# Optimization experiments

Hardware: AMD Instinct MI355X
Metric: run time of the kernel (lower is better)

## Reference

```python
import jax, jax.numpy as jnp
import numpy as np

NUM_NODES = 20000
SEQ_LEN = 128
IN_FEATS = 2
HIDDEN = 32
N_TOTAL = NUM_NODES * SEQ_LEN  # flattened graph size
N_EDGES = 2_000_000


def setup_inputs() -> dict:
    key = jax.random.key(0)
    ks = jax.random.split(key, 10)
    x = jax.random.normal(ks[0], (NUM_NODES, SEQ_LEN, IN_FEATS), dtype=jnp.float32)
    edge_index = jax.random.randint(ks[1], (2, N_EDGES), 0, N_TOTAL, dtype=jnp.int64)
    s = 0.1
    gcn_W = jax.random.normal(ks[2], (IN_FEATS, HIDDEN), dtype=jnp.float32) * s
    gcn_b = jnp.zeros((HIDDEN,), dtype=jnp.float32)
    w_ih = jax.random.normal(ks[3], (4 * HIDDEN, HIDDEN), dtype=jnp.float32) * s
    w_hh = jax.random.normal(ks[4], (4 * HIDDEN, HIDDEN), dtype=jnp.float32) * s
    b_ih = jax.random.normal(ks[5], (4 * HIDDEN,), dtype=jnp.float32) * s
    b_hh = jax.random.normal(ks[6], (4 * HIDDEN,), dtype=jnp.float32) * s
    fc_W = jax.random.normal(ks[7], (HIDDEN, 1), dtype=jnp.float32) * s
    fc_b = jnp.zeros((1,), dtype=jnp.float32)
    return {"x": x, "edge_index": edge_index, "gcn_W": gcn_W, "gcn_b": gcn_b,
            "w_ih": w_ih, "w_hh": w_hh, "b_ih": b_ih, "b_hh": b_hh,
            "fc_W": fc_W, "fc_b": fc_b}


def _gcn(x_flat, edge_index, W, b):
    # PyG GCNConv: add self-loops, symmetric normalization, then linear+bias.
    src, dst = edge_index[0], edge_index[1]
    n = x_flat.shape[0]
    # degree at target side, including the self-loop (+1)
    deg = jax.ops.segment_sum(jnp.ones_like(dst, dtype=x_flat.dtype), dst, num_segments=n) + 1.0
    dinv = jax.lax.rsqrt(deg)  # deg >= 1 always (self-loop)
    h = x_flat @ W  # [n, HIDDEN] transform before propagate
    norm = dinv[src] * dinv[dst]  # [E]
    msg = h[src] * norm[:, None]  # gather + per-edge scale
    agg = jax.ops.segment_sum(msg, dst, num_segments=n)
    # self-loop contribution: dinv_i * dinv_i * h_i = h_i / deg_i
    out = agg + h * (1.0 / deg)[:, None]
    return out + b


def _lstm(xs, w_ih, w_hh, b_ih, b_hh):
    # torch LSTM gate order: i, f, g, o. xs: [N, S, H] -> final hidden [N, H]
    n, s, hdim = xs.shape
    xs_t = jnp.swapaxes(xs, 0, 1)  # [S, N, H]
    # precompute input projections once (dense GEMM)
    x_proj = xs_t @ w_ih.T + b_ih + b_hh  # [S, N, 4H]

    def step(carry, xp):
        h, c = carry
        g = xp + h @ w_hh.T  # [N, 4H]
        i, f, gg, o = jnp.split(g, 4, axis=-1)
        c = jax.nn.sigmoid(f) * c + jax.nn.sigmoid(i) * jnp.tanh(gg)
        h = jax.nn.sigmoid(o) * jnp.tanh(c)
        return (h, c), None

    h0 = jnp.zeros((n, hdim), dtype=xs.dtype)
    (hn, _), _ = jax.lax.scan(step, (h0, h0), x_proj)
    return hn


def reference(x, edge_index, gcn_W, gcn_b, w_ih, w_hh, b_ih, b_hh, fc_W, fc_b):
    num_nodes, seq_len, num_feats = x.shape
    x_in = x.reshape(-1, num_feats)  # [N*S, F]
    x_gcn = jax.nn.relu(_gcn(x_in, edge_index, gcn_W, gcn_b))
    x_lstm = x_gcn.reshape(num_nodes, seq_len, -1)
    hn = _lstm(x_lstm, w_ih, w_hh, b_ih, b_hh)
    return hn @ fc_W + fc_b  # [num_nodes, 1]
```

## Files before the change

### kernel.cpp

```cpp
#include <hip/hip_runtime.h>

#define SEQ 128
#define HID 32

typedef __attribute__((ext_vector_type(8))) short short8;
typedef __attribute__((ext_vector_type(4))) float floatx4;


__global__ void count_kernel(const int* __restrict__ idx, int E, int* __restrict__ cnt) {
    int e = (blockIdx.x * blockDim.x + threadIdx.x) * 4;
    if (((E & 3) == 0) && e + 3 < E) {
        int4 d = *(const int4*)(idx + E + e);
        atomicAdd(&cnt[d.x], 1);
        atomicAdd(&cnt[d.y], 1);
        atomicAdd(&cnt[d.z], 1);
        atomicAdd(&cnt[d.w], 1);
    } else {
        int lim = min(e + 4, E);
        for (int k = e; k < lim; ++k) atomicAdd(&cnt[idx[E + k]], 1);
    }
}

__device__ __forceinline__ unsigned long long pk2(float xx, float yy, float dv) {
    int qx = __float2int_rn(xx * dv * 2097152.0f);
    int qy = __float2int_rn(yy * dv * 2097152.0f);
    return ((unsigned long long)(unsigned)(qx + (1 << 26)) << 32) |
           (unsigned)(qy + (1 << 26));
}

__global__ void scatter_pk_kernel(const int* __restrict__ idx, int E,
                                  const float2* __restrict__ x2,
                                  const int* __restrict__ deg,
                                  unsigned long long* __restrict__ aggP) {
    int e = (blockIdx.x * blockDim.x + threadIdx.x) * 4;
    if (((E & 3) == 0) && e + 3 < E) {
        int4 s = *(const int4*)(idx + e);
        int4 d = *(const int4*)(idx + E + e);
        float2 v0 = x2[s.x];
        float2 v1 = x2[s.y];
        float2 v2 = x2[s.z];
        float2 v3 = x2[s.w];
        float dv0 = rsqrtf((float)deg[s.x] + 1.0f);
        float dv1 = rsqrtf((float)deg[s.y] + 1.0f);
        float dv2 = rsqrtf((float)deg[s.z] + 1.0f);
        float dv3 = rsqrtf((float)deg[s.w] + 1.0f);
        atomicAdd(&aggP[d.x], pk2(v0.x, v0.y, dv0));
        atomicAdd(&aggP[d.y], pk2(v1.x, v1.y, dv1));
        atomicAdd(&aggP[d.z], pk2(v2.x, v2.y, dv2));
        atomicAdd(&aggP[d.w], pk2(v3.x, v3.y, dv3));
    } else {
        int lim = min(e + 4, E);
        for (int k = e; k < lim; ++k) {
            int s = idx[k];
            int d = idx[E + k];
            float2 v = x2[s];
            float dv = rsqrtf((float)deg[s] + 1.0f);
            atomicAdd(&aggP[d], pk2(v.x, v.y, dv));
        }
    }
}


__device__ __forceinline__ float sigm_f(float x) {
    return __builtin_amdgcn_rcpf(1.0f + __expf(-x));
}
__device__ __forceinline__ float tanh_f(float x) {
    return fmaf(__builtin_amdgcn_rcpf(1.0f + __expf(-2.0f * x)), 2.0f, -1.0f);
}
__device__ __forceinline__ void fsplit(float f, short& hi, short& lo) {
    unsigned u = __float_as_uint(f);
    hi = (short)(u >> 16);
    float r = f - __uint_as_float(u & 0xFFFF0000u);
    lo = (short)(__float_as_uint(r) >> 16);
}

__global__ __launch_bounds__(64, 1) void lstm_sw_kernel(
    const float2* __restrict__ x2,
    const unsigned long long* __restrict__ aggP, const int* __restrict__ deg,
    int N,
    const float* __restrict__ gcn_W, const float* __restrict__ gcn_b,
    const float* __restrict__ w_ih, const float* __restrict__ w_hh,
    const float* __restrict__ b_ih, const float* __restrict__ b_hh,
    const float* __restrict__ fc_W, const float* __restrict__ fc_b,
    float* __restrict__ out) {
    __shared__ float2 ubuf[16][SEQ + 1];

    const int lane = threadIdx.x;
    const int n = lane & 15;
    const int qq = lane >> 4;
    const int base = blockIdx.x * 16;

    {
        const float2* xb = x2 + (size_t)base * SEQ;
        const unsigned long long* apb = aggP + (size_t)base * SEQ;
        const int* dgb = deg + (size_t)base * SEQ;
        const int lim = min(16 * SEQ, (N - base) * SEQ);
        #pragma unroll 4
        for (int i = lane; i < 16 * SEQ; i += 64) {
            float2 v = make_float2(0.f, 0.f);
            if (i < lim) {
                int dg = dgb[i];
                float dv = rsqrtf((float)dg + 1.0f);
                float2 xx = xb[i];
                unsigned long long pk = apb[i];
                unsigned bias = (unsigned)dg * 67108864u;
                float ax = (float)((int)((unsigned)(pk >> 32) - bias)) * (1.0f / 2097152.0f);
                float ay = (float)((int)((unsigned)pk - bias)) * (1.0f / 2097152.0f);
                v = make_float2(dv * fmaf(xx.x, dv, ax), dv * fmaf(xx.y, dv, ay));
            }
            ubuf[i >> 7][i & 127] = v;
        }
        if (lane < 16) ubuf[lane][SEQ] = make_float2(0.f, 0.f);
    }

    short8 AiH[4][2], AiL[4][2], AhH[4][2], AhL[4][2];
    floatx4 biasC[4][2];
    #pragma unroll
    for (int g = 0; g < 4; ++g) {
        #pragma unroll
        for (int t1 = 0; t1 < 2; ++t1) {
            const int arow = g * 32 + 8 * (n >> 2) + 4 * t1 + (n & 3);
            const float* wi = w_ih + arow * HID + 8 * qq;
            const float* wh = w_hh + arow * HID + 8 * qq;
            #pragma unroll
            for (int j = 0; j < 8; ++j) {
                short h16, l16;
                fsplit(wi[j], h16, l16); AiH[g][t1][j] = h16; AiL[g][t1][j] = l16;
                fsplit(wh[j], h16, l16); AhH[g][t1][j] = h16; AhL[g][t1][j] = l16;
            }
            #pragma unroll
            for (int r = 0; r < 4; ++r) {
                const int brow = g * 32 + 8 * qq + 4 * t1 + r;
                biasC[g][t1][r] = b_ih[brow] + b_hh[brow];
            }
        }
    }

    float wg0[8], wg1[8], gbc[8], fcw[8];
    #pragma unroll
    for (int j = 0; j < 8; ++j) {
        const int u = 8 * qq + j;
        wg0[j] = gcn_W[u];
        wg1[j] = gcn_W[HID + u];
        gbc[j] = gcn_b[u];
        fcw[j] = fc_W[u];
    }

    float c[2][4], ho[2][4];
    #pragma unroll
    for (int t1 = 0; t1 < 2; ++t1)
        #pragma unroll
        for (int r = 0; r < 4; ++r) { c[t1][r] = 0.f; ho[t1][r] = 0.f; }

    short8 hh = (short8){0, 0, 0, 0, 0, 0, 0, 0};
    short8 hl = (short8){0, 0, 0, 0, 0, 0, 0, 0};
    short8 xh, xl;
    floatx4 aX[4][2];

    {
        float2 uu = ubuf[n][0];
        #pragma unroll
        for (int j = 0; j < 8; ++j) {
            float g = fmaxf(fmaf(uu.x, wg0[j], fmaf(uu.y, wg1[j], gbc[j])), 0.f);
            short h16, l16;
            fsplit(g, h16, l16);
            xh[j] = h16; xl[j] = l16;
        }
    }
    #pragma unroll
    for (int g = 0; g < 4; ++g)
        #pragma unroll
        for (int t1 = 0; t1 < 2; ++t1)
            aX[g][t1] = __builtin_amdgcn_mfma_f32_16x16x32_bf16(AiH[g][t1], xh, biasC[g][t1], 0, 0, 0);
    #pragma unroll
    for (int g = 0; g < 4; ++g)
        #pragma unroll
        for (int t1 = 0; t1 < 2; ++t1)
            aX[g][t1] = __builtin_amdgcn_mfma_f32_16x16x32_bf16(AiL[g][t1], xh, aX[g][t1], 0, 0, 0);
    #pragma unroll
    for (int g = 0; g < 4; ++g)
        #pragma unroll
        for (int t1 = 0; t1 < 2; ++t1)
            aX[g][t1] = __builtin_amdgcn_mfma_f32_16x16x32_bf16(AiH[g][t1], xl, aX[g][t1], 0, 0, 0);

    #pragma unroll 1
    for (int t = 0; t < SEQ; ++t) {
        floatx4 acc[4][2];
        #pragma unroll
        for (int g = 0; g < 4; ++g)
            #pragma unroll
            for (int t1 = 0; t1 < 2; ++t1)
                acc[g][t1] = __builtin_amdgcn_mfma_f32_16x16x32_bf16(AhH[g][t1], hh, aX[g][t1], 0, 0, 0);
        #pragma unroll
        for (int g = 0; g < 4; ++g)
            #pragma unroll
            for (int t1 = 0; t1 < 2; ++t1)
                acc[g][t1] = __builtin_amdgcn_mfma_f32_16x16x32_bf16(AhL[g][t1], hh, acc[g][t1], 0, 0, 0);
        #pragma unroll
        for (int g = 0; g < 4; ++g)
            #pragma unroll
            for (int t1 = 0; t1 < 2; ++t1)
                acc[g][t1] = __builtin_amdgcn_mfma_f32_16x16x32_bf16(AhH[g][t1], hl, acc[g][t1], 0, 0, 0);

        {
            float2 uu = ubuf[n][t + 1];
            #pragma unroll
            for (int j = 0; j < 8; ++j) {
                float g = fmaxf(fmaf(uu.x, wg0[j], fmaf(uu.y, wg1[j], gbc[j])), 0.f);
                short h16, l16;
                fsplit(g, h16, l16);
                xh[j] = h16; xl[j] = l16;
            }
        }
        #pragma unroll
        for (int g = 0; g < 4; ++g)
            #pragma unroll
            for (int t1 = 0; t1 < 2; ++t1)
                aX[g][t1] = __builtin_amdgcn_mfma_f32_16x16x32_bf16(AiH[g][t1], xh, biasC[g][t1], 0, 0, 0);
        #pragma unroll
        for (int g = 0; g < 4; ++g)
            #pragma unroll
            for (int t1 = 0; t1 < 2; ++t1)
                aX[g][t1] = __builtin_amdgcn_mfma_f32_16x16x32_bf16(AiL[g][t1], xh, aX[g][t1], 0, 0, 0);
        #pragma unroll
        for (int g = 0; g < 4; ++g)
            #pragma unroll
            for (int t1 = 0; t1 < 2; ++t1)
                aX[g][t1] = __builtin_amdgcn_mfma_f32_16x16x32_bf16(AiH[g][t1], xl, aX[g][t1], 0, 0, 0);

        #pragma unroll
        for (int t1 = 0; t1 < 2; ++t1) {
            #pragma unroll
            for (int r = 0; r < 4; ++r) {
                const float ig = sigm_f(acc[0][t1][r]);
                const float fg = sigm_f(acc[1][t1][r]);
                const float gg = tanh_f(acc[2][t1][r]);
                const float og = sigm_f(acc[3][t1][r]);
                c[t1][r] = fmaf(fg, c[t1][r], ig * gg);
                const float hv = og * tanh_f(c[t1][r]);
                ho[t1][r] = hv;
                short h16, l16;
                fsplit(hv, h16, l16);
                hh[4 * t1 + r] = h16;
                hl[4 * t1 + r] = l16;
            }
        }
    }

    float partial = 0.f;
    #pragma unroll
    for (int t1 = 0; t1 < 2; ++t1)
        #pragma unroll
        for (int r = 0; r < 4; ++r)
            partial = fmaf(ho[t1][r], fcw[4 * t1 + r], partial);
    partial += __shfl_xor(partial, 16);
    partial += __shfl_xor(partial, 32);
    if (lane < 16) {
        const int node = base + n;
        if (node < N) out[node] = partial + fc_b[0];
    }
}

extern "C" void kernel_launch(void* const* d_in, const int* in_sizes, int n_in,
                              void* d_out, int out_size, void* d_ws, size_t ws_size,
                              hipStream_t stream) {
    const float* x     = (const float*)d_in[0];
    const int*   idx   = (const int*)d_in[1];
    const float* gcn_W = (const float*)d_in[2];
    const float* gcn_b = (const float*)d_in[3];
    const float* w_ih  = (const float*)d_in[4];
    const float* w_hh  = (const float*)d_in[5];
    const float* b_ih  = (const float*)d_in[6];
    const float* b_hh  = (const float*)d_in[7];
    const float* fc_W  = (const float*)d_in[8];
    const float* fc_b  = (const float*)d_in[9];

    const int num_nodes = in_sizes[0] / (SEQ * 2);
    const int ntot = num_nodes * SEQ;
    const int E = in_sizes[1] / 2;

    int* deg = (int*)d_ws;
    unsigned long long* aggP = (unsigned long long*)((char*)d_ws + (size_t)ntot * 4);

    hipMemsetAsync(d_ws, 0, (size_t)ntot * 12, stream);

    const int eb = (E + 1023) / 1024;
    count_kernel<<<eb, 256, 0, stream>>>(idx, E, deg);
    scatter_pk_kernel<<<eb, 256, 0, stream>>>(idx, E, (const float2*)x, deg, aggP);
    lstm_sw_kernel<<<(num_nodes + 15) / 16, 64, 0, stream>>>(
        (const float2*)x, aggP, deg, num_nodes,
        gcn_W, gcn_b, w_ih, w_hh, b_ih, b_hh, fc_W, fc_b,
        (float*)d_out);
}
```

Measured before the change: 542.3 us.

## Split LSTM gates across four waves per block with LDS exchange of state

Each 16-node block now runs four wavefronts instead of one, and each wave computes one gate's MFMA tiles. Gate activations go through shared memory, and each wave updates a 2-hidden-unit slice of the cell and hidden state, written back to LDS for the next step's recurrent MFMA. This cuts the serial MFMA and transcendental chain per step by spreading it over more waves. The cost is two block-wide barriers per timestep plus LDS round trips. MFMA issue is also raised in priority with s_setprio.

```diff
diff --git a/kernel.cpp b/kernel.cpp
--- a/kernel.cpp
+++ b/kernel.cpp
@@ -2,6 +2,8 @@
 
 #define SEQ 128
 #define HID 32
+#define TPB 256
+#define XS 56
 
 typedef __attribute__((ext_vector_type(8))) short short8;
 typedef __attribute__((ext_vector_type(4))) float floatx4;
@@ -73,8 +75,11 @@
     float r = f - __uint_as_float(u & 0xFFFF0000u);
     lo = (short)(__float_as_uint(r) >> 16);
 }
-
-__global__ __launch_bounds__(64, 1) void lstm_sw_kernel(
+__device__ __forceinline__ int pks(short a, short b) {
+    return (int)(((unsigned)(unsigned short)b << 16) | (unsigned short)a);
+}
+
+__global__ __launch_bounds__(TPB, 4) void lstm_gs_kernel(
     const float2* __restrict__ x2,
     const unsigned long long* __restrict__ aggP, const int* __restrict__ deg,
     int N,
@@ -84,10 +89,18 @@
     const float* __restrict__ fc_W, const float* __restrict__ fc_b,
     float* __restrict__ out) {
     __shared__ float2 ubuf[16][SEQ + 1];
-
-    const int lane = threadIdx.x;
+    __shared__ float pre[4][32][17];
+    __shared__ __align__(16) short hhb[16][XS];
+    __shared__ __align__(16) short hlb[16][XS];
+    __shared__ __align__(16) short xgb[16][XS];
+    __shared__ __align__(16) short xlb[16][XS];
+    __shared__ float fcp[4][16];
+
+    const int tid = threadIdx.x;
+    const int w = tid >> 6;
+    const int lane = tid & 63;
     const int n = lane & 15;
-    const int qq = lane >> 4;
+    const int q = lane >> 4;
     const int base = blockIdx.x * 16;
 
     {
@@ -95,8 +108,7 @@
         const unsigned long long* apb = aggP + (size_t)base * SEQ;
         const int* dgb = deg + (size_t)base * SEQ;
         const int lim = min(16 * SEQ, (N - base) * SEQ);
-        #pragma unroll 4
-        for (int i = lane; i < 16 * SEQ; i += 64) {
+        for (int i = tid; i < 16 * SEQ; i += TPB) {
             float2 v = make_float2(0.f, 0.f);
             if (i < lim) {
                 int dg = dgb[i];
@@ -110,154 +122,156 @@
             }
             ubuf[i >> 7][i & 127] = v;
         }
-        if (lane < 16) ubuf[lane][SEQ] = make_float2(0.f, 0.f);
-    }
-
-    short8 AiH[4][2], AiL[4][2], AhH[4][2], AhL[4][2];
-    floatx4 biasC[4][2];
+        if (tid < 16) ubuf[tid][SEQ] = make_float2(0.f, 0.f);
+    }
+
+    short8 AiH[2], AiL[2], AhH[2], AhL[2];
+    floatx4 biasC[2];
     #pragma unroll
-    for (int g = 0; g < 4; ++g) {
-        #pragma unroll
-        for (int t1 = 0; t1 < 2; ++t1) {
-            const int arow = g * 32 + 8 * (n >> 2) + 4 * t1 + (n & 3);
-            const float* wi = w_ih + arow * HID + 8 * qq;
-            const float* wh = w_hh + arow * HID + 8 * qq;
-            #pragma unroll
-            for (int j = 0; j < 8; ++j) {
-                short h16, l16;
-                fsplit(wi[j], h16, l16); AiH[g][t1][j] = h16; AiL[g][t1][j] = l16;
-                fsplit(wh[j], h16, l16); AhH[g][t1][j] = h16; AhL[g][t1][j] = l16;
-            }
-            #pragma unroll
-            for (int r = 0; r < 4; ++r) {
-                const int brow = g * 32 + 8 * qq + 4 * t1 + r;
-                biasC[g][t1][r] = b_ih[brow] + b_hh[brow];
-            }
-        }
-    }
-
-    float wg0[8], wg1[8], gbc[8], fcw[8];
-    #pragma unroll
-    for (int j = 0; j < 8; ++j) {
-        const int u = 8 * qq + j;
-        wg0[j] = gcn_W[u];
-        wg1[j] = gcn_W[HID + u];
-        gbc[j] = gcn_b[u];
-        fcw[j] = fc_W[u];
-    }
-
-    float c[2][4], ho[2][4];
-    #pragma unroll
-    for (int t1 = 0; t1 < 2; ++t1)
-        #pragma unroll
-        for (int r = 0; r < 4; ++r) { c[t1][r] = 0.f; ho[t1][r] = 0.f; }
-
-    short8 hh = (short8){0, 0, 0, 0, 0, 0, 0, 0};
-    short8 hl = (short8){0, 0, 0, 0, 0, 0, 0, 0};
-    short8 xh, xl;
-    floatx4 aX[4][2];
-
+    for (int t1 = 0; t1 < 2; ++t1) {
+        const int arow = w * 32 + 16 * t1 + n;
+        const float* wi = w_ih + arow * HID + 8 * q;
+        const float* wh = w_hh + arow * HID + 8 * q;
+        #pragma unroll
+        for (int j = 0; j < 8; ++j) {
+            short h16, l16;
+            fsplit(wi[j], h16, l16); AiH[t1][j] = h16; AiL[t1][j] = l16;
+            fsplit(wh[j], h16, l16); AhH[t1][j] = h16; AhL[t1][j] = l16;
+        }
+        #pragma unroll
+        for (int r = 0; r < 4; ++r) {
+            const int brow = w * 32 + 16 * t1 + 4 * q + r;
+            biasC[t1][r] = b_ih[brow] + b_hh[brow];
+        }
+    }
+
+    const int ua = 8 * w + 2 * q;
+    const float wg0a = gcn_W[ua],       wg0b = gcn_W[ua + 1];
+    const float wg1a = gcn_W[HID + ua], wg1b = gcn_W[HID + ua + 1];
+    const float gbca = gcn_b[ua],       gbcb = gcn_b[ua + 1];
+    const float fcwa = fc_W[ua],        fcwb = fc_W[ua + 1];
+
+    float c0 = 0.f, c1 = 0.f, ho0 = 0.f, ho1 = 0.f;
+
+    __syncthreads();
+
+    *(int*)&hhb[n][ua] = 0;
+    *(int*)&hlb[n][ua] = 0;
     {
         float2 uu = ubuf[n][0];
-        #pragma unroll
-        for (int j = 0; j < 8; ++j) {
-            float g = fmaxf(fmaf(uu.x, wg0[j], fmaf(uu.y, wg1[j], gbc[j])), 0.f);
-            short h16, l16;
-            fsplit(g, h16, l16);
-            xh[j] = h16; xl[j] = l16;
-        }
-    }
-    #pragma unroll
-    for (int g = 0; g < 4; ++g)
+        float ga = fmaxf(fmaf(uu.x, wg0a, fmaf(uu.y, wg1a, gbca)), 0.f);
+        float gb = fmaxf(fmaf(uu.x, wg0b, fmaf(uu.y, wg1b, gbcb)), 0.f);
+        short gah, gal, gbh, gbl;
+        fsplit(ga, gah, gal); fsplit(gb, gbh, gbl);
+        *(int*)&xgb[n][ua] = pks(gah, gbh);
+        *(int*)&xlb[n][ua] = pks(gal, gbl);
+    }
+    __syncthreads();
+
+    floatx4 aX[2];
+    {
+        const short8 xh = *(const short8*)&xgb[n][8 * q];
+        const short8 xl = *(const short8*)&xlb[n][8 * q];
+        __builtin_amdgcn_s_setprio(1);
         #pragma unroll
         for (int t1 = 0; t1 < 2; ++t1)
-            aX[g][t1] = __builtin_amdgcn_mfma_f32_16x16x32_bf16(AiH[g][t1], xh, biasC[g][t1], 0, 0, 0);
-    #pragma unroll
-    for (int g = 0; g < 4; ++g)
+            aX[t1] = __builtin_amdgcn_mfma_f32_16x16x32_bf16(AiH[t1], xh, biasC[t1], 0, 0, 0);
         #pragma unroll
         for (int t1 = 0; t1 < 2; ++t1)
-            aX[g][t1] = __builtin_amdgcn_mfma_f32_16x16x32_bf16(AiL[g][t1], xh, aX[g][t1], 0, 0, 0);
-    #pragma unroll
-    for (int g = 0; g < 4; ++g)
+            aX[t1] = __builtin_amdgcn_mfma_f32_16x16x32_bf16(AiL[t1], xh, aX[t1], 0, 0, 0);
         #pragma unroll
         for (int t1 = 0; t1 < 2; ++t1)
-            aX[g][t1] = __builtin_amdgcn_mfma_f32_16x16x32_bf16(AiH[g][t1], xl, aX[g][t1], 0, 0, 0);
+            aX[t1] = __builtin_amdgcn_mfma_f32_16x16x32_bf16(AiH[t1], xl, aX[t1], 0, 0, 0);
+        __builtin_amdgcn_s_setprio(0);
+    }
 
     #pragma unroll 1
     for (int t = 0; t < SEQ; ++t) {
-        floatx4 acc[4][2];
-        #pragma unroll
-        for (int g = 0; g < 4; ++g)
-            #pragma unroll
-            for (int t1 = 0; t1 < 2; ++t1)
-                acc[g][t1] = __builtin_amdgcn_mfma_f32_16x16x32_bf16(AhH[g][t1], hh, aX[g][t1], 0, 0, 0);
-        #pragma unroll
-        for (int g = 0; g < 4; ++g)
-            #pragma unroll
-            for (int t1 = 0; t1 < 2; ++t1)
-                acc[g][t1] = __builtin_amdgcn_mfma_f32_16x16x32_bf16(AhL[g][t1], hh, acc[g][t1], 0, 0, 0);
-        #pragma unroll
-        for (int g = 0; g < 4; ++g)
-            #pragma unroll
-            for (int t1 = 0; t1 < 2; ++t1)
-                acc[g][t1] = __builtin_amdgcn_mfma_f32_16x16x32_bf16(AhH[g][t1], hl, acc[g][t1], 0, 0, 0);
-
         {
+            const short8 hh = *(const short8*)&hhb[n][8 * q];
+            const short8 hl = *(const short8*)&hlb[n][8 * q];
+            floatx4 acc[2];
+            __builtin_amdgcn_s_setprio(1);
+            #pragma unroll
+            for (int t1 = 0; t1 < 2; ++t1)
+                acc[t1] = __builtin_amdgcn_mfma_f32_16x16x32_bf16(AhH[t1], hh, aX[t1], 0, 0, 0);
+            #pragma unroll
+            for (int t1 = 0; t1 < 2; ++t1)
+                acc[t1] = __builtin_amdgcn_mfma_f32_16x16x32_bf16(AhL[t1], hh, acc[t1], 0, 0, 0);
+            #pragma unroll
+            for (int t1 = 0; t1 < 2; ++t1)
+                acc[t1] = __builtin_amdgcn_mfma_f32_16x16x32_bf16(AhH[t1], hl, acc[t1], 0, 0, 0);
+            __builtin_amdgcn_s_setprio(0);
+            float av[8];
+            #pragma unroll
+            for (int t1 = 0; t1 < 2; ++t1)
+                #pragma unroll
+                for (int r = 0; r < 4; ++r) av[4 * t1 + r] = acc[t1][r];
+            if (w == 2) {
+                #pragma unroll
+                for (int k = 0; k < 8; ++k) av[k] = tanh_f(av[k]);
+            } else {
+                #pragma unroll
+                for (int k = 0; k < 8; ++k) av[k] = sigm_f(av[k]);
+            }
+            #pragma unroll
+            for (int t1 = 0; t1 < 2; ++t1)
+                #pragma unroll
+                for (int r = 0; r < 4; ++r)
+                    pre[w][16 * t1 + 4 * q + r][n] = av[4 * t1 + r];
+        }
+        __syncthreads();
+
+        {
+            const float i0 = pre[0][ua][n],     f0 = pre[1][ua][n];
+            const float g0 = pre[2][ua][n],     o0 = pre[3][ua][n];
+            const float i1 = pre[0][ua + 1][n], f1 = pre[1][ua + 1][n];
+            const float g1 = pre[2][ua + 1][n], o1 = pre[3][ua + 1][n];
+            c0 = fmaf(f0, c0, i0 * g0);
+            c1 = fmaf(f1, c1, i1 * g1);
+            const float h0 = o0 * tanh_f(c0);
+            const float h1 = o1 * tanh_f(c1);
+            ho0 = h0; ho1 = h1;
+            short h0h, h0l, h1h, h1l;
+            fsplit(h0, h0h, h0l); fsplit(h1, h1h, h1l);
+            *(int*)&hhb[n][ua] = pks(h0h, h1h);
+            *(int*)&hlb[n][ua] = pks(h0l, h1l);
             float2 uu = ubuf[n][t + 1];
-            #pragma unroll
-            for (int j = 0; j < 8; ++j) {
-                float g = fmaxf(fmaf(uu.x, wg0[j], fmaf(uu.y, wg1[j], gbc[j])), 0.f);
-                short h16, l16;
-                fsplit(g, h16, l16);
-                xh[j] = h16; xl[j] = l16;
-            }
-        }
-        #pragma unroll
-        for (int g = 0; g < 4; ++g)
-            #pragma unroll
-            for (int t1 = 0; t1 < 2; ++t1)
-                aX[g][t1] = __builtin_amdgcn_mfma_f32_16x16x32_bf16(AiH[g][t1], xh, biasC[g][t1], 0, 0, 0);
-        #pragma unroll
-        for (int g = 0; g < 4; ++g)
-            #pragma unroll
-            for (int t1 = 0; t1 < 2; ++t1)
-                aX[g][t1] = __builtin_amdgcn_mfma_f32_16x16x32_bf16(AiL[g][t1], xh, aX[g][t1], 0, 0, 0);
-        #pragma unroll
-        for (int g = 0; g < 4; ++g)
-            #pragma unroll
-            for (int t1 = 0; t1 < 2; ++t1)
-                aX[g][t1] = __builtin_amdgcn_mfma_f32_16x16x32_bf16(AiH[g][t1], xl, aX[g][t1], 0, 0, 0);
-
-        #pragma unroll
-        for (int t1 = 0; t1 < 2; ++t1) {
-            #pragma unroll
-            for (int r = 0; r < 4; ++r) {
-                const float ig = sigm_f(acc[0][t1][r]);
-                const float fg = sigm_f(acc[1][t1][r]);
-                const float gg = tanh_f(acc[2][t1][r]);
-                const float og = sigm_f(acc[3][t1][r]);
-                c[t1][r] = fmaf(fg, c[t1][r], ig * gg);
-                const float hv = og * tanh_f(c[t1][r]);
-                ho[t1][r] = hv;
-                short h16, l16;
-                fsplit(hv, h16, l16);
-                hh[4 * t1 + r] = h16;
-                hl[4 * t1 + r] = l16;
-            }
-        }
-    }
-
-    float partial = 0.f;
-    #pragma unroll
-    for (int t1 = 0; t1 < 2; ++t1)
-        #pragma unroll
-        for (int r = 0; r < 4; ++r)
-            partial = fmaf(ho[t1][r], fcw[4 * t1 + r], partial);
+            float ga = fmaxf(fmaf(uu.x, wg0a, fmaf(uu.y, wg1a, gbca)), 0.f);
+            float gb = fmaxf(fmaf(uu.x, wg0b, fmaf(uu.y, wg1b, gbcb)), 0.f);
+            short gah, gal, gbh, gbl;
+            fsplit(ga, gah, gal); fsplit(gb, gbh, gbl);
+            *(int*)&xgb[n][ua] = pks(gah, gbh);
+            *(int*)&xlb[n][ua] = pks(gal, gbl);
+        }
+        __syncthreads();
+
+        {
+            const short8 xh = *(const short8*)&xgb[n][8 * q];
+            const short8 xl = *(const short8*)&xlb[n][8 * q];
+            __builtin_amdgcn_s_setprio(1);
+            #pragma unroll
+            for (int t1 = 0; t1 < 2; ++t1)
+                aX[t1] = __builtin_amdgcn_mfma_f32_16x16x32_bf16(AiH[t1], xh, biasC[t1], 0, 0, 0);
+            #pragma unroll
+            for (int t1 = 0; t1 < 2; ++t1)
+                aX[t1] = __builtin_amdgcn_mfma_f32_16x16x32_bf16(AiL[t1], xh, aX[t1], 0, 0, 0);
+            #pragma unroll
+            for (int t1 = 0; t1 < 2; ++t1)
+                aX[t1] = __builtin_amdgcn_mfma_f32_16x16x32_bf16(AiH[t1], xl, aX[t1], 0, 0, 0);
+            __builtin_amdgcn_s_setprio(0);
+        }
+    }
+
+    float partial = fmaf(ho0, fcwa, ho1 * fcwb);
     partial += __shfl_xor(partial, 16);
     partial += __shfl_xor(partial, 32);
-    if (lane < 16) {
-        const int node = base + n;
-        if (node < N) out[node] = partial + fc_b[0];
+    if (lane < 16) fcp[w][lane] = partial;
+    __syncthreads();
+    if (w == 0 && lane < 16) {
+        const int node = base + lane;
+        if (node < N)
+            out[node] = fcp[0][lane] + fcp[1][lane] + fcp[2][lane] + fcp[3][lane] + fc_b[0];
     }
 }
 
@@ -287,7 +301,7 @@
     const int eb = (E + 1023) / 1024;
     count_kernel<<<eb, 256, 0, stream>>>(idx, E, deg);
     scatter_pk_kernel<<<eb, 256, 0, stream>>>(idx, E, (const float2*)x, deg, aggP);
-    lstm_sw_kernel<<<(num_nodes + 15) / 16, 64, 0, stream>>>(
+    lstm_gs_kernel<<<(num_nodes + 15) / 16, TPB, 0, stream>>>(
         (const float2*)x, aggP, deg, num_nodes,
         gcn_W, gcn_b, w_ih, w_hh, b_ih, b_hh, fc_W, fc_b,
         (float*)d_out);
```

Result: faster. 484.3 us (-10.7%).
